# Optimization experiments

Measured on AMD Instinct MI355X. Metric: run time of the kernel, lower is better.

## Reference

```python
import jax, jax.numpy as jnp
import numpy as np

CUTOFF = 5.0
EPS = 1e-8
N_BASIS = 20
N_LAYERS = 3
F = 128
B, A, N = 4, 256, 64
ZMAX = 100


def _linear(x, W, b=None):
    y = jnp.einsum('...i,oi->...o', x, W)
    return y + b if b is not None else y


def _mlp(x, W1, b1, W2, b2):
    return _linear(jax.nn.silu(_linear(x, W1, b1)), W2, b2)


def _poly_cutoff(d):
    # PolynomialCutoff with p = 6
    p = 6.0
    x = d / CUTOFF
    f = (1.0 - ((p + 1.0) * (p + 2.0) / 2.0) * x**6
         + p * (p + 2.0) * x**7
         - (p * (p + 1.0) / 2.0) * x**8)
    return f * (x < 1.0).astype(d.dtype)


def _rbf(d):
    # RadialBesselLayer: sin(n*pi*d/cutoff) / d, n = 1..N_BASIS
    n = jnp.arange(1, N_BASIS + 1, dtype=d.dtype)
    return jnp.sin(n * jnp.pi * d[..., None] / CUTOFF) / (d[..., None] + EPS)


def _gather(feats, neighbors):
    # feats [B,A,...], neighbors [B,A,N] -> [B,A,N,...]
    return jax.vmap(lambda f, idx: f[idx])(feats, neighbors)


def setup_inputs() -> dict:
    key = jax.random.key(0)
    ks = iter(jax.random.split(key, 64))
    s = 0.08  # weight scale
    inp = {
        'atomic_numbers': jax.random.randint(next(ks), (B, A), 0, ZMAX),
        'positions': jax.random.normal(next(ks), (B, A, 3), jnp.float32),
        'neighbors': jax.random.randint(next(ks), (B, A, N), 0, A),
        'neighbor_mask': jnp.ones((B, A, N), jnp.float32),
        'distances': jax.random.uniform(next(ks), (B, A, N), jnp.float32, 0.1, 4.9),
        'distance_vectors': jax.random.normal(next(ks), (B, A, N, 3), jnp.float32),
        'emb': jax.random.normal(next(ks), (ZMAX, F), jnp.float32) * 0.5,
        'me_W': jax.random.normal(next(ks), (N_LAYERS, F, N_BASIS), jnp.float32) * s,
        'me_b': jnp.zeros((N_LAYERS, F), jnp.float32),
        'mn_W1': jax.random.normal(next(ks), (N_LAYERS, F, F), jnp.float32) * s,
        'mn_b1': jnp.zeros((N_LAYERS, F), jnp.float32),
        'mn_W2': jax.random.normal(next(ks), (N_LAYERS, F, F), jnp.float32) * s,
        'mn_b2': jnp.zeros((N_LAYERS, F), jnp.float32),
        'eqc_W': jax.random.normal(next(ks), (N_LAYERS, 1, F), jnp.float32) * s,
        'eqf_W1': jax.random.normal(next(ks), (N_LAYERS, F, F), jnp.float32) * s,
        'eqf_b1': jnp.zeros((N_LAYERS, F), jnp.float32),
        'eqf_W2': jax.random.normal(next(ks), (N_LAYERS, F, F), jnp.float32) * s,
        'eqf_b2': jnp.zeros((N_LAYERS, F), jnp.float32),
        'esu_W1': jax.random.normal(next(ks), (N_LAYERS, F, F), jnp.float32) * s,
        'esu_b1': jnp.zeros((N_LAYERS, F), jnp.float32),
        'esu_W2': jax.random.normal(next(ks), (N_LAYERS, F, F), jnp.float32) * s,
        'esu_b2': jnp.zeros((N_LAYERS, F), jnp.float32),
        'eme_W1': jax.random.normal(next(ks), (N_LAYERS, F, F), jnp.float32) * s,
        'eme_W2': jax.random.normal(next(ks), (N_LAYERS, F, F), jnp.float32) * s,
        'isu_W1': jax.random.normal(next(ks), (N_LAYERS, F, F), jnp.float32) * s,
        'isu_b1': jnp.zeros((N_LAYERS, F), jnp.float32),
        'isu_W2': jax.random.normal(next(ks), (N_LAYERS, F, F), jnp.float32) * s,
        'isu_b2': jnp.zeros((N_LAYERS, F), jnp.float32),
    }
    return inp


def _forward(atomic_numbers, neighbors, neighbor_mask, distances, distance_vectors,
             emb, me_W, me_b, mn_W1, mn_b1, mn_W2, mn_b2, eqc_W,
             eqf_W1, eqf_b1, eqf_W2, eqf_b2, esu_W1, esu_b1, esu_W2, esu_b2,
             eme_W1, eme_W2, isu_W1, isu_b1, isu_W2, isu_b2):
    # ---- EmbeddingNet ----
    inv_node = emb[atomic_numbers]                      # [B,A,F]
    b, a, f = inv_node.shape
    eq_F = jnp.zeros((b, a, 3), inv_node.dtype)         # [B,A,3]
    eq_f = jnp.zeros((b, a, 3, f), inv_node.dtype)      # [B,A,3,F]
    eq_dr = jnp.zeros((b, a, 3, f), inv_node.dtype)     # [B,A,3,F]
    unit = distance_vectors / (distances[..., None] + EPS)  # [B,A,N,3]
    inv_edge = _rbf(distances)                          # [B,A,N,n_basis]
    cutoff = _poly_cutoff(distances)[..., None]         # [B,A,N,1]
    mask = neighbor_mask[..., None]                     # [B,A,N,1]
    mask2 = neighbor_mask[..., None, None]              # [B,A,N,1,1]

    # ---- InteractionNet x N_LAYERS ----
    for l in range(N_LAYERS):
        msg_edge = _linear(inv_edge, me_W[l], me_b[l]) * cutoff           # [B,A,N,F]
        msg_node = _mlp(inv_node, mn_W1[l], mn_b1[l], mn_W2[l], mn_b2[l])  # [B,A,F]
        msg_node_i = msg_node[:, :, None, :]                               # [B,A,1,F]
        msg_node_f = _gather(msg_node, neighbors)                          # [B,A,N,F]
        inv_msg = msg_edge * msg_node_i * msg_node_f                       # [B,A,N,F]
        # double_update_node = False -> no early invariant update
        eq_msg_F = _linear(inv_msg, eqc_W[l]) * unit                       # [B,A,N,3]
        eq_upd_F = (eq_msg_F * mask).sum(axis=2)                           # [B,A,3]
        eq_F = eq_F + eq_upd_F
        eq_msg_feat = _mlp(inv_msg, eqf_W1[l], eqf_b1[l], eqf_W2[l], eqf_b2[l])
        eq_msg_f = eq_msg_feat[..., None, :] * eq_msg_F[..., None]         # [B,A,N,3,F]
        eq_upd_f = (eq_msg_f * mask2).sum(axis=2)                          # [B,A,3,F]
        eq_f = eq_f + eq_upd_f
        dr_edge = _linear(jax.nn.silu(_linear(inv_msg, eme_W1[l])), eme_W2[l])[..., None, :]  # [B,A,N,1,F]
        dr_node_f = _gather(eq_dr, neighbors)                              # [B,A,N,3,F]
        eq_upd_dr = (dr_edge * dr_node_f * mask2).sum(axis=2)              # [B,A,3,F]
        eq_dr = eq_dr + eq_upd_dr
        eq_dr = eq_dr + _mlp(inv_node, esu_W1[l], esu_b1[l], esu_W2[l], esu_b2[l])[:, :, None, :] * eq_upd_f
        inv_upd = -_mlp(inv_node, isu_W1[l], isu_b1[l], isu_W2[l], isu_b2[l]) * jnp.sum(eq_f * eq_dr, axis=-2)
        inv_node = inv_node + inv_upd
    return inv_node, eq_F, eq_f, eq_dr


def reference(atomic_numbers, positions, neighbors, neighbor_mask, distances, distance_vectors,
              emb, me_W, me_b, mn_W1, mn_b1, mn_W2, mn_b2, eqc_W,
              eqf_W1, eqf_b1, eqf_W2, eqf_b2, esu_W1, esu_b1, esu_W2, esu_b2,
              eme_W1, eme_W2, isu_W1, isu_b1, isu_W2, isu_b2):
    # positions unused (requires_dr = False in EmbeddingNet)
    return _forward(atomic_numbers, neighbors, neighbor_mask, distances, distance_vectors,
                    emb, me_W, me_b, mn_W1, mn_b1, mn_W2, mn_b2, eqc_W,
                    eqf_W1, eqf_b1, eqf_W2, eqf_b2, esu_W1, esu_b1, esu_W2, esu_b2,
                    eme_W1, eme_W2, isu_W1, isu_b1, isu_W2, isu_b2)
```

## Files before the change

kernel.cpp:

```cpp
#include <hip/hip_runtime.h>
#include <cstdint>
#include <cstddef>

#define BB   4
#define AA   256
#define NNB  64
#define FF   128
#define NBAS 20
#define NLAY 3
#define BA   (BB*AA)
#define EDG  (BA*NNB)

typedef __attribute__((ext_vector_type(8))) short bf16x8;
typedef __attribute__((ext_vector_type(4))) float f32x4;

__device__ __forceinline__ float silu_f(float x){ return x / (1.0f + __expf(-x)); }

__device__ __forceinline__ unsigned short f2bf(float x){
  unsigned int u = __float_as_uint(x);
  u += 0x7FFFu + ((u >> 16) & 1u);
  return (unsigned short)(u >> 16);
}
__device__ __forceinline__ unsigned int pk2(float a, float b){
  unsigned int r;
  asm("v_cvt_pk_bf16_f32 %0, %1, %2" : "=v"(r) : "v"(a), "v"(b));
  return r;
}

__device__ __forceinline__ int swzi(int row, int us){
  return (row << 7) + (us ^ ((row & 7) << 3));
}

__global__ void k_cvtw(const float* __restrict__ a, const float* __restrict__ b,
                       const float* __restrict__ c, const float* __restrict__ d,
                       const float* __restrict__ me,
                       const float* __restrict__ mnW1, const float* __restrict__ mnW2,
                       const float* __restrict__ esW1, const float* __restrict__ esW2,
                       const float* __restrict__ isW1, const float* __restrict__ isW2,
                       unsigned short* __restrict__ out){
  int id = blockIdx.x*256 + threadIdx.x;
  if (id < 196608){
    int reg = id / 49152, off = id - reg*49152;
    const float* src = (reg==0)?a:(reg==1)?b:(reg==2)?c:d;
    int lay = off >> 14, us = off & 16383;
    int row = us >> 7, col = us & 127;
    out[id] = f2bf(src[(lay<<14) + (row<<7) + (col ^ ((row&7)<<3))]);
  } else if (id < 208896){
    int p = id - 196608;
    int l = p >> 12;
    int rem = p & 4095;
    int row = rem >> 5, k = rem & 31;
    float v = (k < NBAS) ? me[((size_t)l*FF + row)*NBAS + k] : 0.0f;
    out[id] = f2bf(v);
  } else if (id < 503808){
    int p = id - 208896;
    int mat = p / 49152, rem = p - mat*49152;
    const float* src = (mat==0)?mnW1:(mat==1)?mnW2:(mat==2)?esW1:(mat==3)?esW2:(mat==4)?isW1:isW2;
    out[id] = f2bf(src[rem]);
  }
}

__global__ __launch_bounds__(256) void k_node_mfma(
    const float* __restrict__ X, const int* __restrict__ z,
    const float* __restrict__ emb, float* __restrict__ inv_node,
    const unsigned short* W1a, const float* b1a, const unsigned short* W2a, const float* b2a, float* Ya,
    const unsigned short* W1b, const float* b1b, const unsigned short* W2b, const float* b2b, float* Yb,
    const unsigned short* W1c, const float* b1c, const unsigned short* W2c, const float* b2c, float* Yc,
    int do_emb){
  const unsigned short *W1,*W2; const float *b1,*b2; float* Y;
  if (blockIdx.y==0){ W1=W1a;b1=b1a;W2=W2a;b2=b2a;Y=Ya; }
  else if (blockIdx.y==1){ W1=W1b;b1=b1b;W2=W2b;b2=b2b;Y=Yb; }
  else { W1=W1c;b1=b1c;W2=W2c;b2=b2c;Y=Yc; }
  __shared__ unsigned short Ws[128*136];
  __shared__ unsigned short Xs[64*136];
  const int t = threadIdx.x, w = t>>6, l = t&63;
  const int g = l&15, kg = (l>>4)<<3, r0 = (l>>4)<<2;
  const int gr0 = blockIdx.x*64;
  const int le = w*16 + g;

  {
    int row = t>>2, c0 = (t&3)*32;
    const float* src = do_emb ? (emb + (size_t)z[gr0+row]*FF + c0)
                              : (X   + (size_t)(gr0+row)*FF + c0);
    #pragma unroll
    for (int j=0;j<8;++j){
      float4 v = *(const float4*)(src + j*4);
      if (do_emb && blockIdx.y==0)
        *(float4*)(inv_node + (size_t)(gr0+row)*FF + c0 + j*4) = v;
      uint2 u; u.x = pk2(v.x,v.y); u.y = pk2(v.z,v.w);
      *(uint2*)(&Xs[row*136 + c0 + j*4]) = u;
    }
  }
  #pragma unroll
  for (int c=t; c<2048; c+=256){
    int row = c >> 4, ko = (c & 15) << 3;
    *(int4*)(&Ws[row*136 + ko]) = *(const int4*)(W1 + row*FF + ko);
  }
  __syncthreads();
  bf16x8 xf[4];
  #pragma unroll
  for (int ks=0;ks<4;++ks) xf[ks] = *(const bf16x8*)(&Xs[le*136 + ks*32 + kg]);
  __syncthreads();
  f32x4 acc[8];
  #pragma unroll
  for (int nt=0;nt<8;++nt) acc[nt] = f32x4{0.f,0.f,0.f,0.f};
  #pragma unroll
  for (int nt=0;nt<8;++nt)
    #pragma unroll
    for (int ks=0;ks<4;++ks){
      bf16x8 wfr = *(const bf16x8*)(&Ws[(nt*16+g)*136 + ks*32 + kg]);
      acc[nt] = __builtin_amdgcn_mfma_f32_16x16x32_bf16(wfr, xf[ks], acc[nt], 0,0,0);
    }
  #pragma unroll
  for (int nt=0;nt<8;++nt){
    int o0 = nt*16 + r0;
    float4 bb = *(const float4*)(b1 + o0);
    uint2 u;
    u.x = pk2(silu_f(acc[nt][0]+bb.x), silu_f(acc[nt][1]+bb.y));
    u.y = pk2(silu_f(acc[nt][2]+bb.z), silu_f(acc[nt][3]+bb.w));
    *(uint2*)(&Xs[le*136 + o0]) = u;
  }
  __syncthreads();
  #pragma unroll
  for (int c=t; c<2048; c+=256){
    int row = c >> 4, ko = (c & 15) << 3;
    *(int4*)(&Ws[row*136 + ko]) = *(const int4*)(W2 + row*FF + ko);
  }
  __syncthreads();
  bf16x8 hf[4];
  #pragma unroll
  for (int ks=0;ks<4;++ks) hf[ks] = *(const bf16x8*)(&Xs[le*136 + ks*32 + kg]);
  #pragma unroll
  for (int nt=0;nt<8;++nt) acc[nt] = f32x4{0.f,0.f,0.f,0.f};
  #pragma unroll
  for (int nt=0;nt<8;++nt)
    #pragma unroll
    for (int ks=0;ks<4;++ks){
      bf16x8 wfr = *(const bf16x8*)(&Ws[(nt*16+g)*136 + ks*32 + kg]);
      acc[nt] = __builtin_amdgcn_mfma_f32_16x16x32_bf16(wfr, hf[ks], acc[nt], 0,0,0);
    }
  #pragma unroll
  for (int nt=0;nt<8;++nt){
    int o0 = nt*16 + r0;
    float4 bb = *(const float4*)(b2 + o0);
    float4 o;
    o.x = acc[nt][0]+bb.x; o.y = acc[nt][1]+bb.y;
    o.z = acc[nt][2]+bb.z; o.w = acc[nt][3]+bb.w;
    *(float4*)(Y + (size_t)(gr0 + le)*FF + o0) = o;
  }
}

__device__ __forceinline__ void stage_dma(const unsigned short* Gsw,
                                          unsigned short* buf, int w, int l){
  const char* g = (const char*)Gsw;
  char* bp = (char*)buf;
  #pragma unroll
  for (int i=0;i<8;++i){
    __builtin_amdgcn_global_load_lds(
        (const void*)(g + w*8192 + i*1024 + l*16),
        (void*)(bp + w*8192 + i*1024), 16, 0, 0);
  }
}

__global__ __launch_bounds__(256) void k_layer(
    const float* __restrict__ dist, const float* __restrict__ dvec,
    const float* __restrict__ maskp, const int* __restrict__ nbrs,
    const float* __restrict__ msg_node,
    const unsigned short* __restrict__ meWb, const float* __restrict__ meb,
    const float* __restrict__ eqcW,
    const unsigned short* __restrict__ W1eq, const float* __restrict__ b1eq,
    const unsigned short* __restrict__ W1me,
    const unsigned short* __restrict__ W2eq, const float* __restrict__ b2eq,
    const unsigned short* __restrict__ W2me,
    const float* __restrict__ eqdrT_prev, float* __restrict__ eqdrT_next,
    const float* __restrict__ esu, const float* __restrict__ isu,
    float* __restrict__ eqF, float* __restrict__ eqf_out,
    float* __restrict__ eqdr, float* __restrict__ inv_node, int first){
  __shared__ unsigned short Ws[128*128];
  __shared__ unsigned short Hs[128*128];
  __shared__ float scal[128][4];
  __shared__ int   nbq[128];
  __shared__ float red[4][384];
  __shared__ float eqFred[4][2][3];
  const int t = threadIdx.x, w = t>>6, l = t&63;
  const int bid = blockIdx.x, a0 = bid*2;
  const int g = l&15, kg = (l>>4)<<3, r0 = (l>>4)<<2;
  const float c5 = 0.6283185307179586f;

  stage_dma(W1eq, Hs, w, l);
  if (t < 128){
    int e2 = a0*NNB + t;
    int atomt = a0 + (t>>6);
    nbq[t] = (atomt/AA)*AA + nbrs[e2];
  }

  #pragma unroll
  for (int p=0;p<2;++p){
    const int atom = a0 + p;
    const int eg = atom*NNB + w*16 + g;
    const float d = dist[eg];
    const float dinv = 1.0f/(d + 1e-8f);
    const float xx = d*0.2f;
    float x2=xx*xx, x4=x2*x2, x6=x4*x2, x7=x6*xx, x8=x7*xx;
    float ct = 1.0f - 28.0f*x6 + 48.0f*x7 - 21.0f*x8;
    ct = (xx < 1.0f) ? ct : 0.0f;
    bf16x8 rfr;
    #pragma unroll
    for (int i=0;i<8;++i){
      int k = kg + i;
      float v = (k < NBAS) ? __sinf((float)(k+1)*c5*d)*dinv : 0.0f;
      rfr[i] = (short)f2bf(v);
    }
    f32x4 acc[8];
    #pragma unroll
    for (int nt=0;nt<8;++nt){
      bf16x8 wfr = *(const bf16x8*)(meWb + (nt*16 + g)*32 + kg);
      acc[nt] = __builtin_amdgcn_mfma_f32_16x16x32_bf16(wfr, rfr, f32x4{0.f,0.f,0.f,0.f}, 0,0,0);
    }
    const int bbase = (atom/AA)*AA;
    const int nbv = bbase + nbrs[eg];
    float pv = 0.f;
    #pragma unroll
    for (int nt=0;nt<8;++nt){
      int o0 = nt*16 + r0;
      float4 mb = *(const float4*)(meb + o0);
      float4 mi = *(const float4*)(msg_node + (size_t)atom*FF + o0);
      float4 mf = *(const float4*)(msg_node + (size_t)nbv*FF + o0);
      float4 ec = *(const float4*)(eqcW + o0);
      float v0 = (acc[nt][0]+mb.x)*ct*mi.x*mf.x;
      float v1 = (acc[nt][1]+mb.y)*ct*mi.y*mf.y;
      float v2 = (acc[nt][2]+mb.z)*ct*mi.z*mf.z;
      float v3 = (acc[nt][3]+mb.w)*ct*mi.w*mf.w;
      pv = fmaf(v0,ec.x, fmaf(v1,ec.y, fmaf(v2,ec.z, fmaf(v3,ec.w, pv))));
      uint2 u; u.x = pk2(v0,v1); u.y = pk2(v2,v3);
      *(uint2*)(&Ws[swzi(p*64 + w*16 + g, o0)]) = u;
    }
    pv += __shfl_xor(pv,16); pv += __shfl_xor(pv,32);
    float cf0=0.f, cf1=0.f, cf2=0.f;
    if (l < 16){
      float m  = maskp[eg];
      float s0 = pv*dvec[(size_t)eg*3+0]*dinv;
      float s1 = pv*dvec[(size_t)eg*3+1]*dinv;
      float s2 = pv*dvec[(size_t)eg*3+2]*dinv;
      int lr = p*64 + w*16 + g;
      scal[lr][0]=s0; scal[lr][1]=s1; scal[lr][2]=s2; scal[lr][3]=m;
      cf0 = s0*m; cf1 = s1*m; cf2 = s2*m;
    }
    #pragma unroll
    for (int s2=1; s2<16; s2<<=1){
      cf0 += __shfl_xor(cf0,s2); cf1 += __shfl_xor(cf1,s2); cf2 += __shfl_xor(cf2,s2);
    }
    if (l == 0){ eqFred[w][p][0]=cf0; eqFred[w][p][1]=cf1; eqFred[w][p][2]=cf2; }
  }
  __syncthreads();

  bf16x8 xf[2][4];
  #pragma unroll
  for (int ms=0;ms<2;++ms)
    #pragma unroll
    for (int ks=0;ks<4;++ks)
      xf[ms][ks] = *(const bf16x8*)(&Ws[swzi(w*32 + ms*16 + g, ks*32 + kg)]);
  if (t < 6){
    int p = t/3, c = t - p*3;
    float s = eqFred[0][p][c]+eqFred[1][p][c]+eqFred[2][p][c]+eqFred[3][p][c];
    eqF[(a0+p)*3 + c] = first ? s : (eqF[(a0+p)*3 + c] + s);
  }
  __syncthreads();

  f32x4 acc2[2][8];
  #pragma unroll
  for (int ms=0;ms<2;++ms)
    #pragma unroll
    for (int nt=0;nt<8;++nt) acc2[ms][nt] = f32x4{0.f,0.f,0.f,0.f};
  #pragma unroll
  for (int nt=0;nt<8;++nt)
    #pragma unroll
    for (int ks=0;ks<4;++ks){
      bf16x8 wfr = *(const bf16x8*)(&Hs[swzi(nt*16+g, ks*32+kg)]);
      #pragma unroll
      for (int ms=0;ms<2;++ms)
        acc2[ms][nt] = __builtin_amdgcn_mfma_f32_16x16x32_bf16(wfr, xf[ms][ks], acc2[ms][nt], 0,0,0);
    }
  __syncthreads();
  stage_dma(W2eq, Hs, w, l);
  #pragma unroll
  for (int ms=0;ms<2;++ms)
    #pragma unroll
    for (int nt=0;nt<8;++nt){
      int o0 = nt*16 + r0;
      float4 bb = *(const float4*)(b1eq + o0);
      uint2 u;
      u.x = pk2(silu_f(acc2[ms][nt][0]+bb.x), silu_f(acc2[ms][nt][1]+bb.y));
      u.y = pk2(silu_f(acc2[ms][nt][2]+bb.z), silu_f(acc2[ms][nt][3]+bb.w));
      *(uint2*)(&Ws[swzi(w*32 + ms*16 + g, o0)]) = u;
    }
  __syncthreads();

  {
    bf16x8 hfr[2][4];
    #pragma unroll
    for (int ms=0;ms<2;++ms)
      #pragma unroll
      for (int ks=0;ks<4;++ks)
        hfr[ms][ks] = *(const bf16x8*)(&Ws[swzi(w*32 + ms*16 + g, ks*32 + kg)]);
    #pragma unroll
    for (int ms=0;ms<2;++ms)
      #pragma unroll
      for (int nt=0;nt<8;++nt) acc2[ms][nt] = f32x4{0.f,0.f,0.f,0.f};
    #pragma unroll
    for (int nt=0;nt<8;++nt)
      #pragma unroll
      for (int ks=0;ks<4;++ks){
        bf16x8 wfr = *(const bf16x8*)(&Hs[swzi(nt*16+g, ks*32+kg)]);
        #pragma unroll
        for (int ms=0;ms<2;++ms)
          acc2[ms][nt] = __builtin_amdgcn_mfma_f32_16x16x32_bf16(hfr[ms][ks], wfr, acc2[ms][nt], 0,0,0);
      }
    #pragma unroll
    for (int nt=0;nt<8;++nt){
      int col = nt*16 + g;
      float bb = b2eq[col];
      float q0=0.f,q1=0.f,q2=0.f;
      #pragma unroll
      for (int ms=0;ms<2;++ms)
        #pragma unroll
        for (int r=0;r<4;++r){
          int row = w*32 + ms*16 + r0 + r;
          float ym = (acc2[ms][nt][r] + bb) * scal[row][3];
          q0 = fmaf(ym, scal[row][0], q0);
          q1 = fmaf(ym, scal[row][1], q1);
          q2 = fmaf(ym, scal[row][2], q2);
        }
      q0 += __shfl_xor(q0,16); q0 += __shfl_xor(q0,32);
      q1 += __shfl_xor(q1,16); q1 += __shfl_xor(q1,32);
      q2 += __shfl_xor(q2,16); q2 += __shfl_xor(q2,32);
      if (l < 16){
        red[w][0*128+col] = q0; red[w][1*128+col] = q1; red[w][2*128+col] = q2;
      }
    }
  }
  __syncthreads();

  if (!first) stage_dma(W1me, Ws, w, l);

  float ef_reg[3], s1_reg[3];
  {
    int k = 0;
    for (int i=t; i<768; i+=256, ++k){
      int p = (i >= 384) ? 1 : 0;
      int j = i - p*384;
      float s1 = red[2*p][j] + red[2*p+1][j];
      size_t idx = (size_t)(a0+p)*384 + j;
      float ef = first ? s1 : (eqf_out[idx] + s1);
      eqf_out[idx] = ef;
      ef_reg[k] = ef; s1_reg[k] = s1;
    }
  }
  __syncthreads();

  if (!first){
    #pragma unroll
    for (int ms=0;ms<2;++ms)
      #pragma unroll
      for (int nt=0;nt<8;++nt) acc2[ms][nt] = f32x4{0.f,0.f,0.f,0.f};
    #pragma unroll
    for (int nt=0;nt<8;++nt)
      #pragma unroll
      for (int ks=0;ks<4;++ks){
        bf16x8 wfr = *(const bf16x8*)(&Ws[swzi(nt*16+g, ks*32+kg)]);
        #pragma unroll
        for (int ms=0;ms<2;++ms)
          acc2[ms][nt] = __builtin_amdgcn_mfma_f32_16x16x32_bf16(wfr, xf[ms][ks], acc2[ms][nt], 0,0,0);
      }
    __syncthreads();
    stage_dma(W2me, Ws, w, l);
    #pragma unroll
    for (int ms=0;ms<2;++ms)
      #pragma unroll
      for (int nt=0;nt<8;++nt){
        int o0 = nt*16 + r0;
        uint2 u;
        u.x = pk2(silu_f(acc2[ms][nt][0]), silu_f(acc2[ms][nt][1]));
        u.y = pk2(silu_f(acc2[ms][nt][2]), silu_f(acc2[ms][nt][3]));
        *(uint2*)(&Hs[swzi(w*32 + ms*16 + g, o0)]) = u;
      }
    __syncthreads();
    bf16x8 hfr[2][4];
    #pragma unroll
    for (int ms=0;ms<2;++ms)
      #pragma unroll
      for (int ks=0;ks<4;++ks)
        hfr[ms][ks] = *(const bf16x8*)(&Hs[swzi(w*32 + ms*16 + g, ks*32 + kg)]);
    #pragma unroll
    for (int ms=0;ms<2;++ms)
      #pragma unroll
      for (int nt=0;nt<8;++nt) acc2[ms][nt] = f32x4{0.f,0.f,0.f,0.f};
    #pragma unroll
    for (int nt=0;nt<8;++nt)
      #pragma unroll
      for (int ks=0;ks<4;++ks){
        bf16x8 wfr = *(const bf16x8*)(&Ws[swzi(nt*16+g, ks*32+kg)]);
        #pragma unroll
        for (int ms=0;ms<2;++ms)
          acc2[ms][nt] = __builtin_amdgcn_mfma_f32_16x16x32_bf16(hfr[ms][ks], wfr, acc2[ms][nt], 0,0,0);
      }
    #pragma unroll
    for (int nt=0;nt<8;++nt){
      int col = nt*16 + g;
      float q0=0.f,q1=0.f,q2=0.f;
      #pragma unroll
      for (int ms=0;ms<2;++ms)
        #pragma unroll
        for (int r=0;r<4;++r){
          int row = w*32 + ms*16 + r0 + r;
          float ym = acc2[ms][nt][r] * scal[row][3];
          float4 gv = *(const float4*)(eqdrT_prev + ((size_t)nbq[row]*FF + col)*4);
          q0 = fmaf(ym, gv.x, q0);
          q1 = fmaf(ym, gv.y, q1);
          q2 = fmaf(ym, gv.z, q2);
        }
      q0 += __shfl_xor(q0,16); q0 += __shfl_xor(q0,32);
      q1 += __shfl_xor(q1,16); q1 += __shfl_xor(q1,32);
      q2 += __shfl_xor(q2,16); q2 += __shfl_xor(q2,32);
      if (l < 16){
        red[w][0*128+col] = q0; red[w][1*128+col] = q1; red[w][2*128+col] = q2;
      }
    }
    __syncthreads();
  }

  {
    int k = 0;
    for (int i=t; i<768; i+=256, ++k){
      int p = (i >= 384) ? 1 : 0;
      int j = i - p*384;
      int o = j & 127;
      int c = j >> 7;
      float s2 = first ? 0.0f : (red[2*p][j] + red[2*p+1][j]);
      size_t idx = (size_t)(a0+p)*384 + j;
      float es = esu[(size_t)(a0+p)*FF + o];
      float v = (first ? 0.0f : eqdr[idx]) + s2 + es*s1_reg[k];
      eqdr[idx] = v;
      eqdrT_next[((size_t)(a0+p)*FF + o)*4 + c] = v;
      red[2*p][j] = ef_reg[k] * v;
    }
  }
  __syncthreads();
  {
    int p = t >> 7, o = t & 127;
    float sum3 = red[2*p][o] + red[2*p][128+o] + red[2*p][256+o];
    size_t idx = (size_t)(a0+p)*FF + o;
    inv_node[idx] = fmaf(-isu[idx], sum3, inv_node[idx]);
  }
}

extern "C" void kernel_launch(void* const* d_in, const int* in_sizes, int n_in,
                              void* d_out, int out_size, void* d_ws, size_t ws_size,
                              hipStream_t stream){
  const int*   z     = (const int*)  d_in[0];
  const int*   nbrs  = (const int*)  d_in[2];
  const float* maskp = (const float*)d_in[3];
  const float* dist  = (const float*)d_in[4];
  const float* dvec  = (const float*)d_in[5];
  const float* emb   = (const float*)d_in[6];
  const float* me_W  = (const float*)d_in[7];
  const float* me_b  = (const float*)d_in[8];
  const float* mn_W1 = (const float*)d_in[9];
  const float* mn_b1 = (const float*)d_in[10];
  const float* mn_W2 = (const float*)d_in[11];
  const float* mn_b2 = (const float*)d_in[12];
  const float* eqc_W = (const float*)d_in[13];
  const float* eqf_W1= (const float*)d_in[14];
  const float* eqf_b1= (const float*)d_in[15];
  const float* eqf_W2= (const float*)d_in[16];
  const float* eqf_b2= (const float*)d_in[17];
  const float* esu_W1= (const float*)d_in[18];
  const float* esu_b1= (const float*)d_in[19];
  const float* esu_W2= (const float*)d_in[20];
  const float* esu_b2= (const float*)d_in[21];
  const float* eme_W1= (const float*)d_in[22];
  const float* eme_W2= (const float*)d_in[23];
  const float* isu_W1= (const float*)d_in[24];
  const float* isu_b1= (const float*)d_in[25];
  const float* isu_W2= (const float*)d_in[26];
  const float* isu_b2= (const float*)d_in[27];

  float* out      = (float*)d_out;
  float* inv_node = out;
  float* eqF      = out + 131072;
  float* eqf      = out + 134144;
  float* eqdr     = out + 527360;

  float* w        = (float*)d_ws;
  float* msg_node = w;
  float* esu_o    = w + 131072;
  float* isu_o    = w + 262144;
  float* eqdrT_A  = w + 393216;
  float* eqdrT_B  = w + 917504;
  unsigned short* wbf = (unsigned short*)(w + 1441792);

  k_cvtw<<<1968, 256, 0, stream>>>(eqf_W1, eqf_W2, eme_W1, eme_W2, me_W,
      mn_W1, mn_W2, esu_W1, esu_W2, isu_W1, isu_W2, wbf);

  const unsigned short* mnW1b0  = wbf + 208896;
  const unsigned short* mnW2b0  = wbf + 258048;
  const unsigned short* esW1b0  = wbf + 307200;
  const unsigned short* esW2b0  = wbf + 356352;
  const unsigned short* isW1b0  = wbf + 405504;
  const unsigned short* isW2b0  = wbf + 454656;

  k_node_mfma<<<dim3(BA/64, 3), 256, 0, stream>>>(nullptr, z, emb, inv_node,
      mnW1b0, mn_b1,  mnW2b0, mn_b2,  msg_node,
      esW1b0, esu_b1, esW2b0, esu_b2, esu_o,
      isW1b0, isu_b1, isW2b0, isu_b2, isu_o, 1);

  for (int l=0; l<NLAY; ++l){
    size_t oB = (size_t)l*FF;
    const unsigned short* eqfW1b = wbf + 0*49152 + l*16384;
    const unsigned short* eqfW2b = wbf + 1*49152 + l*16384;
    const unsigned short* emeW1b = wbf + 2*49152 + l*16384;
    const unsigned short* emeW2b = wbf + 3*49152 + l*16384;
    const unsigned short* meWb   = wbf + 196608  + l*4096;
    float* dT_prev = (l & 1) ? eqdrT_B : eqdrT_A;
    float* dT_next = (l & 1) ? eqdrT_A : eqdrT_B;
    int first = (l==0);

    k_layer<<<BA/2, 256, 0, stream>>>(dist, dvec, maskp, nbrs, msg_node,
        meWb, me_b+oB, eqc_W+oB,
        eqfW1b, eqf_b1+oB, emeW1b,
        eqfW2b, eqf_b2+oB, emeW2b,
        dT_prev, dT_next, esu_o, isu_o,
        eqF, eqf, eqdr, inv_node, first);
    if (l < NLAY-1){
      size_t oBn = (size_t)(l+1)*FF;
      k_node_mfma<<<dim3(BA/64, 3), 256, 0, stream>>>(inv_node, nullptr, nullptr, nullptr,
          mnW1b0 + (l+1)*16384, mn_b1+oBn,  mnW2b0 + (l+1)*16384, mn_b2+oBn,  msg_node,
          esW1b0 + (l+1)*16384, esu_b1+oBn, esW2b0 + (l+1)*16384, esu_b2+oBn, esu_o,
          isW1b0 + (l+1)*16384, isu_b1+oBn, isW2b0 + (l+1)*16384, isu_b2+oBn, isu_o, 0);
    }
  }
}
```

Measured before the change: 134.5 us.

## Double k_layer block to 512 threads, one 16-edge row tile per wave

The per-layer kernel now runs 8 waves per block instead of 4. Each wave handles 16 edge rows instead of 32, so the two-m-subtile loops, register fragments and accumulators are halved, and the DMA weight staging, reductions and shared buffers are re-partitioned for 8 waves. The aim is more parallelism and latency hiding with fewer registers per thread, at the cost of more waves contending for the same shared memory and barriers, and a 4-way instead of 2-way partial reduction.

```diff
diff --git a/kernel.cpp b/kernel.cpp
--- a/kernel.cpp
+++ b/kernel.cpp
@@ -155,14 +155,14 @@
   const char* g = (const char*)Gsw;
   char* bp = (char*)buf;
   #pragma unroll
-  for (int i=0;i<8;++i){
+  for (int i=0;i<4;++i){
     __builtin_amdgcn_global_load_lds(
-        (const void*)(g + w*8192 + i*1024 + l*16),
-        (void*)(bp + w*8192 + i*1024), 16, 0, 0);
-  }
-}
-
-__global__ __launch_bounds__(256) void k_layer(
+        (const void*)(g + w*4096 + i*1024 + l*16),
+        (void*)(bp + w*4096 + i*1024), 16, 0, 0);
+  }
+}
+
+__global__ __launch_bounds__(512) void k_layer(
     const float* __restrict__ dist, const float* __restrict__ dvec,
     const float* __restrict__ maskp, const int* __restrict__ nbrs,
     const float* __restrict__ msg_node,
@@ -180,11 +180,13 @@
   __shared__ unsigned short Hs[128*128];
   __shared__ float scal[128][4];
   __shared__ int   nbq[128];
-  __shared__ float red[4][384];
-  __shared__ float eqFred[4][2][3];
+  __shared__ float red[8][384];
+  __shared__ float eqFred[8][3];
   const int t = threadIdx.x, w = t>>6, l = t&63;
   const int bid = blockIdx.x, a0 = bid*2;
   const int g = l&15, kg = (l>>4)<<3, r0 = (l>>4)<<2;
+  const int p  = w>>2;
+  const int le = w*16 + g;
   const float c5 = 0.6283185307179586f;
 
   stage_dma(W1eq, Hs, w, l);
@@ -194,10 +196,9 @@
     nbq[t] = (atomt/AA)*AA + nbrs[e2];
   }
 
-  #pragma unroll
-  for (int p=0;p<2;++p){
+  {
     const int atom = a0 + p;
-    const int eg = atom*NNB + w*16 + g;
+    const int eg = atom*NNB + (w&3)*16 + g;
     const float d = dist[eg];
     const float dinv = 1.0f/(d + 1e-8f);
     const float xx = d*0.2f;
@@ -233,7 +234,7 @@
       float v3 = (acc[nt][3]+mb.w)*ct*mi.w*mf.w;
       pv = fmaf(v0,ec.x, fmaf(v1,ec.y, fmaf(v2,ec.z, fmaf(v3,ec.w, pv))));
       uint2 u; u.x = pk2(v0,v1); u.y = pk2(v2,v3);
-      *(uint2*)(&Ws[swzi(p*64 + w*16 + g, o0)]) = u;
+      *(uint2*)(&Ws[swzi(le, o0)]) = u;
     }
     pv += __shfl_xor(pv,16); pv += __shfl_xor(pv,32);
     float cf0=0.f, cf1=0.f, cf2=0.f;
@@ -242,79 +243,64 @@
       float s0 = pv*dvec[(size_t)eg*3+0]*dinv;
       float s1 = pv*dvec[(size_t)eg*3+1]*dinv;
       float s2 = pv*dvec[(size_t)eg*3+2]*dinv;
-      int lr = p*64 + w*16 + g;
-      scal[lr][0]=s0; scal[lr][1]=s1; scal[lr][2]=s2; scal[lr][3]=m;
+      scal[le][0]=s0; scal[le][1]=s1; scal[le][2]=s2; scal[le][3]=m;
       cf0 = s0*m; cf1 = s1*m; cf2 = s2*m;
     }
     #pragma unroll
     for (int s2=1; s2<16; s2<<=1){
       cf0 += __shfl_xor(cf0,s2); cf1 += __shfl_xor(cf1,s2); cf2 += __shfl_xor(cf2,s2);
     }
-    if (l == 0){ eqFred[w][p][0]=cf0; eqFred[w][p][1]=cf1; eqFred[w][p][2]=cf2; }
-  }
-  __syncthreads();
-
-  bf16x8 xf[2][4];
-  #pragma unroll
-  for (int ms=0;ms<2;++ms)
-    #pragma unroll
-    for (int ks=0;ks<4;++ks)
-      xf[ms][ks] = *(const bf16x8*)(&Ws[swzi(w*32 + ms*16 + g, ks*32 + kg)]);
+    if (l == 0){ eqFred[w][0]=cf0; eqFred[w][1]=cf1; eqFred[w][2]=cf2; }
+  }
+  __syncthreads();
+
+  bf16x8 xf[4];
+  #pragma unroll
+  for (int ks=0;ks<4;++ks)
+    xf[ks] = *(const bf16x8*)(&Ws[swzi(le, ks*32 + kg)]);
   if (t < 6){
-    int p = t/3, c = t - p*3;
-    float s = eqFred[0][p][c]+eqFred[1][p][c]+eqFred[2][p][c]+eqFred[3][p][c];
-    eqF[(a0+p)*3 + c] = first ? s : (eqF[(a0+p)*3 + c] + s);
-  }
-  __syncthreads();
-
-  f32x4 acc2[2][8];
-  #pragma unroll
-  for (int ms=0;ms<2;++ms)
-    #pragma unroll
-    for (int nt=0;nt<8;++nt) acc2[ms][nt] = f32x4{0.f,0.f,0.f,0.f};
+    int pp = t/3, c = t - pp*3;
+    float s = eqFred[4*pp][c]+eqFred[4*pp+1][c]+eqFred[4*pp+2][c]+eqFred[4*pp+3][c];
+    eqF[(a0+pp)*3 + c] = first ? s : (eqF[(a0+pp)*3 + c] + s);
+  }
+  __syncthreads();
+
+  f32x4 acc2[8];
+  #pragma unroll
+  for (int nt=0;nt<8;++nt) acc2[nt] = f32x4{0.f,0.f,0.f,0.f};
   #pragma unroll
   for (int nt=0;nt<8;++nt)
     #pragma unroll
     for (int ks=0;ks<4;++ks){
       bf16x8 wfr = *(const bf16x8*)(&Hs[swzi(nt*16+g, ks*32+kg)]);
-      #pragma unroll
-      for (int ms=0;ms<2;++ms)
-        acc2[ms][nt] = __builtin_amdgcn_mfma_f32_16x16x32_bf16(wfr, xf[ms][ks], acc2[ms][nt], 0,0,0);
+      acc2[nt] = __builtin_amdgcn_mfma_f32_16x16x32_bf16(wfr, xf[ks], acc2[nt], 0,0,0);
     }
   __syncthreads();
   stage_dma(W2eq, Hs, w, l);
   #pragma unroll
-  for (int ms=0;ms<2;++ms)
-    #pragma unroll
-    for (int nt=0;nt<8;++nt){
-      int o0 = nt*16 + r0;
-      float4 bb = *(const float4*)(b1eq + o0);
-      uint2 u;
-      u.x = pk2(silu_f(acc2[ms][nt][0]+bb.x), silu_f(acc2[ms][nt][1]+bb.y));
-      u.y = pk2(silu_f(acc2[ms][nt][2]+bb.z), silu_f(acc2[ms][nt][3]+bb.w));
-      *(uint2*)(&Ws[swzi(w*32 + ms*16 + g, o0)]) = u;
-    }
+  for (int nt=0;nt<8;++nt){
+    int o0 = nt*16 + r0;
+    float4 bb = *(const float4*)(b1eq + o0);
+    uint2 u;
+    u.x = pk2(silu_f(acc2[nt][0]+bb.x), silu_f(acc2[nt][1]+bb.y));
+    u.y = pk2(silu_f(acc2[nt][2]+bb.z), silu_f(acc2[nt][3]+bb.w));
+    *(uint2*)(&Ws[swzi(le, o0)]) = u;
+  }
   __syncthreads();
 
   {
-    bf16x8 hfr[2][4];
-    #pragma unroll
-    for (int ms=0;ms<2;++ms)
-      #pragma unroll
-      for (int ks=0;ks<4;++ks)
-        hfr[ms][ks] = *(const bf16x8*)(&Ws[swzi(w*32 + ms*16 + g, ks*32 + kg)]);
-    #pragma unroll
-    for (int ms=0;ms<2;++ms)
-      #pragma unroll
-      for (int nt=0;nt<8;++nt) acc2[ms][nt] = f32x4{0.f,0.f,0.f,0.f};
+    bf16x8 hfr[4];
+    #pragma unroll
+    for (int ks=0;ks<4;++ks)
+      hfr[ks] = *(const bf16x8*)(&Ws[swzi(le, ks*32 + kg)]);
+    #pragma unroll
+    for (int nt=0;nt<8;++nt) acc2[nt] = f32x4{0.f,0.f,0.f,0.f};
     #pragma unroll
     for (int nt=0;nt<8;++nt)
       #pragma unroll
       for (int ks=0;ks<4;++ks){
         bf16x8 wfr = *(const bf16x8*)(&Hs[swzi(nt*16+g, ks*32+kg)]);
-        #pragma unroll
-        for (int ms=0;ms<2;++ms)
-          acc2[ms][nt] = __builtin_amdgcn_mfma_f32_16x16x32_bf16(hfr[ms][ks], wfr, acc2[ms][nt], 0,0,0);
+        acc2[nt] = __builtin_amdgcn_mfma_f32_16x16x32_bf16(hfr[ks], wfr, acc2[nt], 0,0,0);
       }
     #pragma unroll
     for (int nt=0;nt<8;++nt){
@@ -322,15 +308,13 @@
       float bb = b2eq[col];
       float q0=0.f,q1=0.f,q2=0.f;
       #pragma unroll
-      for (int ms=0;ms<2;++ms)
-        #pragma unroll
-        for (int r=0;r<4;++r){
-          int row = w*32 + ms*16 + r0 + r;
-          float ym = (acc2[ms][nt][r] + bb) * scal[row][3];
-          q0 = fmaf(ym, scal[row][0], q0);
-          q1 = fmaf(ym, scal[row][1], q1);
-          q2 = fmaf(ym, scal[row][2], q2);
-        }
+      for (int r=0;r<4;++r){
+        int row = w*16 + r0 + r;
+        float ym = (acc2[nt][r] + bb) * scal[row][3];
+        q0 = fmaf(ym, scal[row][0], q0);
+        q1 = fmaf(ym, scal[row][1], q1);
+        q2 = fmaf(ym, scal[row][2], q2);
+      }
       q0 += __shfl_xor(q0,16); q0 += __shfl_xor(q0,32);
       q1 += __shfl_xor(q1,16); q1 += __shfl_xor(q1,32);
       q2 += __shfl_xor(q2,16); q2 += __shfl_xor(q2,32);
@@ -343,14 +327,14 @@
 
   if (!first) stage_dma(W1me, Ws, w, l);
 
-  float ef_reg[3], s1_reg[3];
+  float ef_reg[2], s1_reg[2];
   {
     int k = 0;
-    for (int i=t; i<768; i+=256, ++k){
-      int p = (i >= 384) ? 1 : 0;
-      int j = i - p*384;
-      float s1 = red[2*p][j] + red[2*p+1][j];
-      size_t idx = (size_t)(a0+p)*384 + j;
+    for (int i=t; i<768; i+=512, ++k){
+      int pp = (i >= 384) ? 1 : 0;
+      int j = i - pp*384;
+      float s1 = red[4*pp][j] + red[4*pp+1][j] + red[4*pp+2][j] + red[4*pp+3][j];
+      size_t idx = (size_t)(a0+pp)*384 + j;
       float ef = first ? s1 : (eqf_out[idx] + s1);
       eqf_out[idx] = ef;
       ef_reg[k] = ef; s1_reg[k] = s1;
@@ -360,65 +344,51 @@
 
   if (!first){
     #pragma unroll
-    for (int ms=0;ms<2;++ms)
-      #pragma unroll
-      for (int nt=0;nt<8;++nt) acc2[ms][nt] = f32x4{0.f,0.f,0.f,0.f};
+    for (int nt=0;nt<8;++nt) acc2[nt] = f32x4{0.f,0.f,0.f,0.f};
     #pragma unroll
     for (int nt=0;nt<8;++nt)
       #pragma unroll
       for (int ks=0;ks<4;++ks){
         bf16x8 wfr = *(const bf16x8*)(&Ws[swzi(nt*16+g, ks*32+kg)]);
-        #pragma unroll
-        for (int ms=0;ms<2;++ms)
-          acc2[ms][nt] = __builtin_amdgcn_mfma_f32_16x16x32_bf16(wfr, xf[ms][ks], acc2[ms][nt], 0,0,0);
+        acc2[nt] = __builtin_amdgcn_mfma_f32_16x16x32_bf16(wfr, xf[ks], acc2[nt], 0,0,0);
       }
     __syncthreads();
     stage_dma(W2me, Ws, w, l);
     #pragma unroll
-    for (int ms=0;ms<2;++ms)
-      #pragma unroll
-      for (int nt=0;nt<8;++nt){
-        int o0 = nt*16 + r0;
-        uint2 u;
-        u.x = pk2(silu_f(acc2[ms][nt][0]), silu_f(acc2[ms][nt][1]));
-        u.y = pk2(silu_f(acc2[ms][nt][2]), silu_f(acc2[ms][nt][3]));
-        *(uint2*)(&Hs[swzi(w*32 + ms*16 + g, o0)]) = u;
-      }
+    for (int nt=0;nt<8;++nt){
+      int o0 = nt*16 + r0;
+      uint2 u;
+      u.x = pk2(silu_f(acc2[nt][0]), silu_f(acc2[nt][1]));
+      u.y = pk2(silu_f(acc2[nt][2]), silu_f(acc2[nt][3]));
+      *(uint2*)(&Hs[swzi(le, o0)]) = u;
+    }
     __syncthreads();
-    bf16x8 hfr[2][4];
-    #pragma unroll
-    for (int ms=0;ms<2;++ms)
-      #pragma unroll
-      for (int ks=0;ks<4;++ks)
-        hfr[ms][ks] = *(const bf16x8*)(&Hs[swzi(w*32 + ms*16 + g, ks*32 + kg)]);
-    #pragma unroll
-    for (int ms=0;ms<2;++ms)
-      #pragma unroll
-      for (int nt=0;nt<8;++nt) acc2[ms][nt] = f32x4{0.f,0.f,0.f,0.f};
+    bf16x8 hfr[4];
+    #pragma unroll
+    for (int ks=0;ks<4;++ks)
+      hfr[ks] = *(const bf16x8*)(&Hs[swzi(le, ks*32 + kg)]);
+    #pragma unroll
+    for (int nt=0;nt<8;++nt) acc2[nt] = f32x4{0.f,0.f,0.f,0.f};
     #pragma unroll
     for (int nt=0;nt<8;++nt)
       #pragma unroll
       for (int ks=0;ks<4;++ks){
         bf16x8 wfr = *(const bf16x8*)(&Ws[swzi(nt*16+g, ks*32+kg)]);
-        #pragma unroll
-        for (int ms=0;ms<2;++ms)
-          acc2[ms][nt] = __builtin_amdgcn_mfma_f32_16x16x32_bf16(hfr[ms][ks], wfr, acc2[ms][nt], 0,0,0);
+        acc2[nt] = __builtin_amdgcn_mfma_f32_16x16x32_bf16(hfr[ks], wfr, acc2[nt], 0,0,0);
       }
     #pragma unroll
     for (int nt=0;nt<8;++nt){
       int col = nt*16 + g;
       float q0=0.f,q1=0.f,q2=0.f;
       #pragma unroll
-      for (int ms=0;ms<2;++ms)
-        #pragma unroll
-        for (int r=0;r<4;++r){
-          int row = w*32 + ms*16 + r0 + r;
-          float ym = acc2[ms][nt][r] * scal[row][3];
-          float4 gv = *(const float4*)(eqdrT_prev + ((size_t)nbq[row]*FF + col)*4);
-          q0 = fmaf(ym, gv.x, q0);
-          q1 = fmaf(ym, gv.y, q1);
-          q2 = fmaf(ym, gv.z, q2);
-        }
+      for (int r=0;r<4;++r){
+        int row = w*16 + r0 + r;
+        float ym = acc2[nt][r] * scal[row][3];
+        float4 gv = *(const float4*)(eqdrT_prev + ((size_t)nbq[row]*FF + col)*4);
+        q0 = fmaf(ym, gv.x, q0);
+        q1 = fmaf(ym, gv.y, q1);
+        q2 = fmaf(ym, gv.z, q2);
+      }
       q0 += __shfl_xor(q0,16); q0 += __shfl_xor(q0,32);
       q1 += __shfl_xor(q1,16); q1 += __shfl_xor(q1,32);
       q2 += __shfl_xor(q2,16); q2 += __shfl_xor(q2,32);
@@ -431,25 +401,25 @@
 
   {
     int k = 0;
-    for (int i=t; i<768; i+=256, ++k){
-      int p = (i >= 384) ? 1 : 0;
-      int j = i - p*384;
+    for (int i=t; i<768; i+=512, ++k){
+      int pp = (i >= 384) ? 1 : 0;
+      int j = i - pp*384;
       int o = j & 127;
       int c = j >> 7;
-      float s2 = first ? 0.0f : (red[2*p][j] + red[2*p+1][j]);
-      size_t idx = (size_t)(a0+p)*384 + j;
-      float es = esu[(size_t)(a0+p)*FF + o];
+      float s2 = first ? 0.0f : (red[4*pp][j] + red[4*pp+1][j] + red[4*pp+2][j] + red[4*pp+3][j]);
+      size_t idx = (size_t)(a0+pp)*384 + j;
+      float es = esu[(size_t)(a0+pp)*FF + o];
       float v = (first ? 0.0f : eqdr[idx]) + s2 + es*s1_reg[k];
       eqdr[idx] = v;
-      eqdrT_next[((size_t)(a0+p)*FF + o)*4 + c] = v;
-      red[2*p][j] = ef_reg[k] * v;
-    }
-  }
-  __syncthreads();
-  {
-    int p = t >> 7, o = t & 127;
-    float sum3 = red[2*p][o] + red[2*p][128+o] + red[2*p][256+o];
-    size_t idx = (size_t)(a0+p)*FF + o;
+      eqdrT_next[((size_t)(a0+pp)*FF + o)*4 + c] = v;
+      red[4*pp][j] = ef_reg[k] * v;
+    }
+  }
+  __syncthreads();
+  if (t < 256){
+    int pp = t >> 7, o = t & 127;
+    float sum3 = red[4*pp][o] + red[4*pp][128+o] + red[4*pp][256+o];
+    size_t idx = (size_t)(a0+pp)*FF + o;
     inv_node[idx] = fmaf(-isu[idx], sum3, inv_node[idx]);
   }
 }
@@ -525,7 +495,7 @@
     float* dT_next = (l & 1) ? eqdrT_A : eqdrT_B;
     int first = (l==0);
 
-    k_layer<<<BA/2, 256, 0, stream>>>(dist, dvec, maskp, nbrs, msg_node,
+    k_layer<<<BA/2, 512, 0, stream>>>(dist, dvec, maskp, nbrs, msg_node,
         meWb, me_b+oB, eqc_W+oB,
         eqfW1b, eqf_b1+oB, emeW1b,
         eqfW2b, eqf_b2+oB, emeW2b,
```

Measured after the change: 166.3 us. 1.24x slower.
